# Kernel tuning notes

Hardware: AMD Instinct MI355X
Metric: run time of the kernel (lower is better)

The kernel has to match this reference:

```python
import jax, jax.numpy as jnp
import numpy as np
from jax import lax

N_NODES = 50000
N_EDGES = 1_600_000
BATCH = 4
T_STEPS = 50
DT = 0.02  # integration step (s)


def setup_inputs() -> dict:
    key = jax.random.key(0)
    ks = jax.random.split(key, 8)
    x = jax.random.normal(ks[0], (BATCH, T_STEPS, N_NODES), jnp.float32) * 0.5
    # NeuronBias: normal(mean=0.5, std=0.05)
    bias = (jax.random.normal(ks[1], (N_NODES,), jnp.float32) * 0.05 + 0.5)
    # NeuronTimeConst: around 0.05s, kept positive
    time_const = jax.random.uniform(ks[2], (N_NODES,), jnp.float32) * 0.045 + 0.005
    # EdgeSign: +/-1
    sign = jnp.where(jax.random.uniform(ks[3], (N_EDGES,)) < 0.5, -1.0, 1.0).astype(jnp.float32)
    # SynCount: lognormal, non-negative
    syn_count = jnp.exp(jax.random.normal(ks[4], (N_EDGES,), jnp.float32) * 0.5)
    # SynStrength: small positive scale (scale_chem/scale_elec = 0.01)
    syn_strength = jax.random.uniform(ks[5], (N_EDGES,), jnp.float32) * 0.01
    src_idx = jax.random.randint(ks[6], (N_EDGES,), 0, N_NODES, dtype=jnp.int32)
    tgt_idx = jax.random.randint(ks[7], (N_EDGES,), 0, N_NODES, dtype=jnp.int32)
    return dict(x=x, bias=bias, time_const=time_const, sign=sign,
                syn_count=syn_count, syn_strength=syn_strength,
                src_idx=src_idx, tgt_idx=tgt_idx)


def reference(x, bias, time_const, sign, syn_count, syn_strength, src_idx, tgt_idx):
    """Recurrent connectome dynamics (StaticSynapses, relu activation).

    Per step: gather relu(v) at source nodes, weight each edge by
    sign*syn_count*syn_strength, scatter-add into target nodes, then Euler
    update v += dt/tau * (-v + bias + synaptic_input + stimulus).
    Returns relu(v) over time: [B, T, N].
    """
    B, T, N = x.shape
    # clamp configs: non_negative on counts/strengths
    weight = sign * jax.nn.relu(syn_count) * jax.nn.relu(syn_strength)  # [E]
    tau = jnp.maximum(time_const, DT)
    alpha = DT / tau  # [N]

    v0 = jnp.broadcast_to(bias, (B, N))  # initial state at bias

    def step(v, x_t):
        rates = jax.nn.relu(v)                      # [B, N]
        msg = rates[:, src_idx] * weight            # gather -> edge transform [B, E]
        summed = jnp.zeros((B, N), x.dtype).at[:, tgt_idx].add(msg)  # scatter-reduce
        v_new = v + alpha * (-v + bias + summed + x_t)
        return v_new, jax.nn.relu(v_new)

    _, out = lax.scan(step, v0, jnp.moveaxis(x, 1, 0))  # scan over T
    return jnp.moveaxis(out, 0, 1)  # [B, T, N]
```

## Files before the change

kernel.cpp:

```cpp
#include <hip/hip_runtime.h>
#include <hip/hip_fp16.h>

#define N_NODES 50000
#define N_EDGES 1600000
#define T_STEPS 50
#define DT      0.02f
#define NB      256
#define NPB     196
#define CAP     6912
#define CAP2    7168
#define TILE    4096
#define G       8


__global__ __launch_bounds__(256) void zero_kernel(int* __restrict__ bucket_count) {
    bucket_count[threadIdx.x] = 0;
}

__global__ __launch_bounds__(256) void bucket_kernel(
    const int* __restrict__ src, const int* __restrict__ tgt,
    const float* __restrict__ sign, const float* __restrict__ syn_count,
    const float* __restrict__ syn_strength,
    int* __restrict__ bucket_count, unsigned long long* __restrict__ rec_buf)
{
    __shared__ int hist[NB], base_s[NB], cur[NB];
    int tid = threadIdx.x;
    hist[tid] = 0;
    __syncthreads();

    int e0 = blockIdx.x * TILE + tid;
    int bkt[16];
    unsigned long long item[16];
#pragma unroll
    for (int k = 0; k < 16; ++k) {
        int e = e0 + k * 256;
        if (e < N_EDGES) {
            int t = tgt[e];
            int b = t / NPB;
            int tl = t - b * NPB;
            float w = sign[e] * fmaxf(syn_count[e], 0.f) * fmaxf(syn_strength[e], 0.f);
            unsigned int rec = (unsigned int)src[e] |
                               ((unsigned int)__half_as_ushort(__float2half(w)) << 16);
            bkt[k] = b;
            item[k] = (unsigned long long)rec | ((unsigned long long)tl << 32);
            atomicAdd(&hist[b], 1);
        } else {
            bkt[k] = -1;
        }
    }
    __syncthreads();
    base_s[tid] = atomicAdd(&bucket_count[tid], hist[tid]);
    cur[tid] = 0;
    __syncthreads();
#pragma unroll
    for (int k = 0; k < 16; ++k) {
        if (bkt[k] >= 0) {
            int p = base_s[bkt[k]] + atomicAdd(&cur[bkt[k]], 1);
            if (p < CAP) rec_buf[(size_t)bkt[k] * CAP + p] = item[k];
        }
    }
}

__global__ __launch_bounds__(256) void sort_kernel(
    const int* __restrict__ bucket_count,
    const unsigned long long* __restrict__ rec_buf,
    const float* __restrict__ bias, const float* __restrict__ time_const,
    unsigned int* __restrict__ edges_g,
    int* __restrict__ offsets, int* __restrict__ ends,
    float2* __restrict__ ab, float* __restrict__ v ,
    uint2* __restrict__ rates0 )
{
    __shared__ unsigned int sorted[CAP2];
    __shared__ int loc_off[NPB + 1];
    __shared__ int loc_cnt[NPB];
    __shared__ int loc_cur[NPB];

    int b = blockIdx.x;
    int tid = threadIdx.x;
    int node_base = b * NPB;
    int n_nodes = min(NPB, N_NODES - node_base);
    int ebase = b * CAP2;
    int cnt = min(bucket_count[b], CAP);

    for (int i = tid; i < CAP2; i += 256) sorted[i] = 0;
    if (tid < NPB) loc_cnt[tid] = 0;
    __syncthreads();

    for (int i = tid; i < cnt; i += 256) {
        unsigned long long it = rec_buf[(size_t)b * CAP + i];
        atomicAdd(&loc_cnt[(int)(it >> 32)], 1);
    }
    __syncthreads();
    if (tid == 0) {
        int r = 0;
        for (int n = 0; n < n_nodes; ++n) {
            loc_off[n] = r;
            r += (loc_cnt[n] + 1) & ~1;
        }
        loc_off[n_nodes] = r;
    }
    __syncthreads();
    if (tid < n_nodes) loc_cur[tid] = loc_off[tid];
    __syncthreads();

    for (int i = tid; i < cnt; i += 256) {
        unsigned long long it = rec_buf[(size_t)b * CAP + i];
        int p = atomicAdd(&loc_cur[(int)(it >> 32)], 1);
        sorted[p] = (unsigned int)it;
    }
    __syncthreads();

    int total = loc_off[n_nodes];
    for (int i = tid; i < total; i += 256) edges_g[ebase + i] = sorted[i];
    for (int n = tid; n < n_nodes; n += 256) {
        int gn = node_base + n;
        offsets[gn] = ebase + loc_off[n];
        ends[gn]    = ebase + loc_off[n + 1];
        float bb  = bias[gn];
        float tau = fmaxf(time_const[gn], DT);
        ab[gn] = make_float2(DT / tau, bb);
        v[gn] = bb; v[N_NODES + gn] = bb;
        v[2 * N_NODES + gn] = bb; v[3 * N_NODES + gn] = bb;
        __half hr = __float2half(fmaxf(bb, 0.f));
        __half2 h2 = __halves2half2(hr, hr);
        uint2 r0; r0.x = *(unsigned int*)&h2; r0.y = r0.x;
        rates0[gn] = r0;
    }
}

__device__ __forceinline__ float rec_w(unsigned int rec) {
    return __half2float(__ushort_as_half((unsigned short)(rec >> 16)));
}
__device__ __forceinline__ float4 h4_to_f4(uint2 g) {
    __half2 h01 = *(__half2*)&g.x;
    __half2 h23 = *(__half2*)&g.y;
    float2 f01 = __half22float2(h01);
    float2 f23 = __half22float2(h23);
    return make_float4(f01.x, f01.y, f23.x, f23.y);
}

__global__ __launch_bounds__(256) void step_kernel(
    const uint2* __restrict__ rates_in ,
    __half* __restrict__ rates_out ,
    float* __restrict__ v ,
    const float2* __restrict__ ab,
    const int* __restrict__ offsets, const int* __restrict__ ends,
    const unsigned int* __restrict__ edges,
    const float* __restrict__ x, float* __restrict__ out, int t, int nblk)
{
    int nb8 = nblk / 8;
    int idx = blockIdx.x;
    int node_block = (idx < nb8 * 8) ? (idx % 8) * nb8 + idx / 8 : idx;
    int node = node_block * (256 / G) + ((int)threadIdx.x / G);
    int lane = threadIdx.x & (G - 1);
    if (node >= N_NODES) return;

    int beg = offsets[node], end = ends[node];
    float4 acc = make_float4(0.f, 0.f, 0.f, 0.f);

    const uint2 zz = make_uint2(0u, 0u);
    int i = beg + 2 * lane;
    uint2 p0 = (i          < end) ? *(const uint2*)(edges + i)          : zz;
    uint2 p1 = (i + 2 * G  < end) ? *(const uint2*)(edges + i + 2 * G)  : zz;
    while (i < end) {
        uint2 q0 = (i + 4 * G < end) ? *(const uint2*)(edges + i + 4 * G) : zz;
        uint2 q1 = (i + 6 * G < end) ? *(const uint2*)(edges + i + 6 * G) : zz;
        float4 a0 = h4_to_f4(rates_in[p0.x & 0xFFFFu]);
        float4 a1 = h4_to_f4(rates_in[p0.y & 0xFFFFu]);
        float4 a2 = h4_to_f4(rates_in[p1.x & 0xFFFFu]);
        float4 a3 = h4_to_f4(rates_in[p1.y & 0xFFFFu]);
        float w0 = rec_w(p0.x), w1 = rec_w(p0.y), w2 = rec_w(p1.x), w3 = rec_w(p1.y);
        acc.x = fmaf(a0.x, w0, acc.x); acc.y = fmaf(a0.y, w0, acc.y);
        acc.z = fmaf(a0.z, w0, acc.z); acc.w = fmaf(a0.w, w0, acc.w);
        acc.x = fmaf(a1.x, w1, acc.x); acc.y = fmaf(a1.y, w1, acc.y);
        acc.z = fmaf(a1.z, w1, acc.z); acc.w = fmaf(a1.w, w1, acc.w);
        acc.x = fmaf(a2.x, w2, acc.x); acc.y = fmaf(a2.y, w2, acc.y);
        acc.z = fmaf(a2.z, w2, acc.z); acc.w = fmaf(a2.w, w2, acc.w);
        acc.x = fmaf(a3.x, w3, acc.x); acc.y = fmaf(a3.y, w3, acc.y);
        acc.z = fmaf(a3.z, w3, acc.z); acc.w = fmaf(a3.w, w3, acc.w);
        p0 = q0; p1 = q1;
        i += 4 * G;
    }

#pragma unroll
    for (int m = 1; m < G; m <<= 1) {
        acc.x += __shfl_xor(acc.x, m, 64);
        acc.y += __shfl_xor(acc.y, m, 64);
        acc.z += __shfl_xor(acc.z, m, 64);
        acc.w += __shfl_xor(acc.w, m, 64);
    }

    if (lane < 4) {
        float sum = (lane == 0) ? acc.x : (lane == 1) ? acc.y
                  : (lane == 2) ? acc.z : acc.w;
        float2 abv = ab[node];
        const int TN = T_STEPS * N_NODES;
        int vi = lane * N_NODES + node;
        int oi = lane * TN + t * N_NODES + node;
        float vv = v[vi];
        float xv = __builtin_nontemporal_load(x + oi);
        float vn = vv + abv.x * (abv.y + sum + xv - vv);
        v[vi] = vn;
        float r = fmaxf(vn, 0.f);
        rates_out[node * 4 + lane] = __float2half(r);
        __builtin_nontemporal_store(r, out + oi);
    }
}


extern "C" void kernel_launch(void* const* d_in, const int* in_sizes, int n_in,
                              void* d_out, int out_size, void* d_ws, size_t ws_size,
                              hipStream_t stream) {
    const float* x            = (const float*)d_in[0];
    const float* bias         = (const float*)d_in[1];
    const float* time_const   = (const float*)d_in[2];
    const float* sign         = (const float*)d_in[3];
    const float* syn_count    = (const float*)d_in[4];
    const float* syn_strength = (const float*)d_in[5];
    const int*   src_idx      = (const int*)d_in[6];
    const int*   tgt_idx      = (const int*)d_in[7];
    float* out = (float*)d_out;

    char* ws = (char*)d_ws;
    size_t off = 0;
    auto alloc = [&](size_t bytes) -> void* {
        void* p = ws + off;
        off = (off + bytes + 255) & ~(size_t)255;
        return p;
    };
    float*  v       = (float*) alloc((size_t)N_NODES * 4 * 4);
    uint2*  rates_a = (uint2*) alloc((size_t)N_NODES * 8);
    uint2*  rates_b = (uint2*) alloc((size_t)N_NODES * 8);
    float2* ab      = (float2*)alloc((size_t)N_NODES * 8);
    int*    offsets = (int*)   alloc((size_t)N_NODES * 4);
    int*    ends    = (int*)   alloc((size_t)N_NODES * 4);
    int*    bucket_count = (int*)alloc((size_t)NB * 4);
    unsigned int* edges = (unsigned int*)alloc((size_t)NB * CAP2 * 4);
    unsigned long long* rec_buf =
        (unsigned long long*)alloc((size_t)NB * CAP * 8);

    int nb_tiles = (N_EDGES + TILE - 1) / TILE;

    zero_kernel<<<1, 256, 0, stream>>>(bucket_count);
    bucket_kernel<<<nb_tiles, 256, 0, stream>>>(src_idx, tgt_idx, sign, syn_count,
                                                syn_strength, bucket_count, rec_buf);
    sort_kernel<<<NB, 256, 0, stream>>>(bucket_count, rec_buf, bias, time_const,
                                        edges, offsets, ends, ab, v, rates_a);

    int nblk = (N_NODES + (256 / G) - 1) / (256 / G);
    for (int t = 0; t < T_STEPS; ++t) {
        const uint2* rin  = (t & 1) ? rates_b : rates_a;
        __half*      rout = (__half*)((t & 1) ? rates_a : rates_b);
        step_kernel<<<nblk, 256, 0, stream>>>(rin, rout, v, ab,
                                              offsets, ends, edges, x, out, t, nblk);
    }
}
```

Measured before the change: 788.9 us.

## Stage source-rate chunks in LDS and sort edges by source chunk per node

The sort pass now groups each target node's edges by source-node chunk (8 chunks of 6250 nodes) and records per-chunk offsets. The step kernel becomes 256 blocks of 1024 threads, each with 4 lanes per node. Each block streams the rate array chunk by chunk into shared memory, with register double-buffering, and gathers from LDS instead of global memory. This swaps random global gathers for coalesced loads, but every block reloads the full rate array each step, adds many barriers, and leaves only 256 blocks with little parallelism per node.

```diff
diff --git a/kernel.cpp b/kernel.cpp
--- a/kernel.cpp
+++ b/kernel.cpp
@@ -8,9 +8,10 @@
 #define NB      256
 #define NPB     196
 #define CAP     6912
-#define CAP2    7168
 #define TILE    4096
-#define G       8
+#define NCH     8
+#define CHUNK   6250
+#define SREG    7
 
 
 __global__ __launch_bounds__(256) void zero_kernel(int* __restrict__ bucket_count) {
@@ -65,57 +66,57 @@
     const int* __restrict__ bucket_count,
     const unsigned long long* __restrict__ rec_buf,
     const float* __restrict__ bias, const float* __restrict__ time_const,
-    unsigned int* __restrict__ edges_g,
-    int* __restrict__ offsets, int* __restrict__ ends,
+    unsigned int* __restrict__ edges_g, int* __restrict__ co,
     float2* __restrict__ ab, float* __restrict__ v ,
     uint2* __restrict__ rates0 )
 {
-    __shared__ unsigned int sorted[CAP2];
-    __shared__ int loc_off[NPB + 1];
-    __shared__ int loc_cnt[NPB];
-    __shared__ int loc_cur[NPB];
-
-    int b = blockIdx.x;
-    int tid = threadIdx.x;
+    __shared__ unsigned int sorted[CAP];
+    __shared__ int kcnt[NPB * NCH];
+    __shared__ int kcur[NPB * NCH];
+    __shared__ int nsum[256];
+
+    int b = blockIdx.x, tid = threadIdx.x;
     int node_base = b * NPB;
     int n_nodes = min(NPB, N_NODES - node_base);
-    int ebase = b * CAP2;
+    int ebase = b * CAP;
     int cnt = min(bucket_count[b], CAP);
 
-    for (int i = tid; i < CAP2; i += 256) sorted[i] = 0;
-    if (tid < NPB) loc_cnt[tid] = 0;
+    for (int i = tid; i < NPB * NCH; i += 256) kcnt[i] = 0;
     __syncthreads();
 
     for (int i = tid; i < cnt; i += 256) {
         unsigned long long it = rec_buf[(size_t)b * CAP + i];
-        atomicAdd(&loc_cnt[(int)(it >> 32)], 1);
-    }
-    __syncthreads();
-    if (tid == 0) {
-        int r = 0;
-        for (int n = 0; n < n_nodes; ++n) {
-            loc_off[n] = r;
-            r += (loc_cnt[n] + 1) & ~1;
-        }
-        loc_off[n_nodes] = r;
-    }
-    __syncthreads();
-    if (tid < n_nodes) loc_cur[tid] = loc_off[tid];
-    __syncthreads();
-
-    for (int i = tid; i < cnt; i += 256) {
-        unsigned long long it = rec_buf[(size_t)b * CAP + i];
-        int p = atomicAdd(&loc_cur[(int)(it >> 32)], 1);
-        sorted[p] = (unsigned int)it;
-    }
-    __syncthreads();
-
-    int total = loc_off[n_nodes];
-    for (int i = tid; i < total; i += 256) edges_g[ebase + i] = sorted[i];
-    for (int n = tid; n < n_nodes; n += 256) {
-        int gn = node_base + n;
-        offsets[gn] = ebase + loc_off[n];
-        ends[gn]    = ebase + loc_off[n + 1];
+        int tl = (int)(it >> 32);
+        int c  = (int)((unsigned int)it & 0xFFFFu) / CHUNK;
+        atomicAdd(&kcnt[tl * NCH + c], 1);
+    }
+    __syncthreads();
+
+    int my_tot = 0;
+    if (tid < NPB) {
+#pragma unroll
+        for (int k = 0; k < NCH; ++k) my_tot += kcnt[tid * NCH + k];
+    }
+    nsum[tid] = my_tot;
+    __syncthreads();
+    for (int off = 1; off < 256; off <<= 1) {
+        int val = (tid >= off) ? nsum[tid - off] : 0;
+        __syncthreads();
+        nsum[tid] += val;
+        __syncthreads();
+    }
+
+    if (tid < n_nodes) {
+        int run = (tid == 0) ? 0 : nsum[tid - 1];
+        int gn = node_base + tid;
+#pragma unroll
+        for (int k = 0; k < NCH; ++k) {
+            kcur[tid * NCH + k] = run;
+            co[gn * (NCH + 1) + k] = ebase + run;
+            run += kcnt[tid * NCH + k];
+        }
+        co[gn * (NCH + 1) + NCH] = ebase + run;
+
         float bb  = bias[gn];
         float tau = fmaxf(time_const[gn], DT);
         ab[gn] = make_float2(DT / tau, bb);
@@ -126,6 +127,18 @@
         uint2 r0; r0.x = *(unsigned int*)&h2; r0.y = r0.x;
         rates0[gn] = r0;
     }
+    __syncthreads();
+
+    for (int i = tid; i < cnt; i += 256) {
+        unsigned long long it = rec_buf[(size_t)b * CAP + i];
+        int tl = (int)(it >> 32);
+        int c  = (int)((unsigned int)it & 0xFFFFu) / CHUNK;
+        int p = atomicAdd(&kcur[tl * NCH + c], 1);
+        sorted[p] = (unsigned int)it;
+    }
+    __syncthreads();
+
+    for (int i = tid; i < cnt; i += 256) edges_g[ebase + i] = sorted[i];
 }
 
 __device__ __forceinline__ float rec_w(unsigned int rec) {
@@ -139,71 +152,96 @@
     return make_float4(f01.x, f01.y, f23.x, f23.y);
 }
 
-__global__ __launch_bounds__(256) void step_kernel(
+__global__ __launch_bounds__(1024) void step_kernel(
     const uint2* __restrict__ rates_in ,
     __half* __restrict__ rates_out ,
     float* __restrict__ v ,
     const float2* __restrict__ ab,
-    const int* __restrict__ offsets, const int* __restrict__ ends,
-    const unsigned int* __restrict__ edges,
-    const float* __restrict__ x, float* __restrict__ out, int t, int nblk)
+    const int* __restrict__ co, const unsigned int* __restrict__ edges,
+    const float* __restrict__ x, float* __restrict__ out, int t)
 {
-    int nb8 = nblk / 8;
-    int idx = blockIdx.x;
-    int node_block = (idx < nb8 * 8) ? (idx % 8) * nb8 + idx / 8 : idx;
-    int node = node_block * (256 / G) + ((int)threadIdx.x / G);
-    int lane = threadIdx.x & (G - 1);
-    if (node >= N_NODES) return;
-
-    int beg = offsets[node], end = ends[node];
+    __shared__ uint2 lds_r[CHUNK];
+
+    int b = blockIdx.x, tid = threadIdx.x;
+    int node_base = b * NPB;
+    int n_nodes = min(NPB, N_NODES - node_base);
+    int group = tid >> 2, lane = tid & 3;
+    bool active = group < n_nodes;
+    int gn = node_base + group;
     float4 acc = make_float4(0.f, 0.f, 0.f, 0.f);
 
-    const uint2 zz = make_uint2(0u, 0u);
-    int i = beg + 2 * lane;
-    uint2 p0 = (i          < end) ? *(const uint2*)(edges + i)          : zz;
-    uint2 p1 = (i + 2 * G  < end) ? *(const uint2*)(edges + i + 2 * G)  : zz;
-    while (i < end) {
-        uint2 q0 = (i + 4 * G < end) ? *(const uint2*)(edges + i + 4 * G) : zz;
-        uint2 q1 = (i + 6 * G < end) ? *(const uint2*)(edges + i + 6 * G) : zz;
-        float4 a0 = h4_to_f4(rates_in[p0.x & 0xFFFFu]);
-        float4 a1 = h4_to_f4(rates_in[p0.y & 0xFFFFu]);
-        float4 a2 = h4_to_f4(rates_in[p1.x & 0xFFFFu]);
-        float4 a3 = h4_to_f4(rates_in[p1.y & 0xFFFFu]);
-        float w0 = rec_w(p0.x), w1 = rec_w(p0.y), w2 = rec_w(p1.x), w3 = rec_w(p1.y);
+    int off9[NCH + 1];
+    if (active) {
+#pragma unroll
+        for (int k = 0; k <= NCH; ++k) off9[k] = co[gn * (NCH + 1) + k];
+    } else {
+#pragma unroll
+        for (int k = 0; k <= NCH; ++k) off9[k] = 0;
+    }
+
+    uint2 st[SREG];
+#pragma unroll
+    for (int k = 0; k < SREG; ++k) {
+        int i = tid + k * 1024;
+        st[k] = (i < CHUNK) ? rates_in[i] : make_uint2(0u, 0u);
+    }
+
+    for (int c = 0; c < NCH; ++c) {
+        __syncthreads();
+#pragma unroll
+        for (int k = 0; k < SREG; ++k) {
+            int i = tid + k * 1024;
+            if (i < CHUNK) lds_r[i] = st[k];
+        }
+        if (c + 1 < NCH) {
+            const uint2* nxt = rates_in + (c + 1) * CHUNK;
+#pragma unroll
+            for (int k = 0; k < SREG; ++k) {
+                int i = tid + k * 1024;
+                st[k] = (i < CHUNK) ? nxt[i] : make_uint2(0u, 0u);
+            }
+        }
+        __syncthreads();
+
+        int beg = off9[c], end = off9[c + 1];
+        int cb = c * CHUNK;
+        int i = beg + lane;
+        unsigned int r0 = (i     < end) ? edges[i]     : (unsigned int)cb;
+        unsigned int r1 = (i + 4 < end) ? edges[i + 4] : (unsigned int)cb;
+        float4 a0 = h4_to_f4(lds_r[(int)(r0 & 0xFFFFu) - cb]);
+        float4 a1 = h4_to_f4(lds_r[(int)(r1 & 0xFFFFu) - cb]);
+        float w0 = rec_w(r0), w1 = rec_w(r1);
         acc.x = fmaf(a0.x, w0, acc.x); acc.y = fmaf(a0.y, w0, acc.y);
         acc.z = fmaf(a0.z, w0, acc.z); acc.w = fmaf(a0.w, w0, acc.w);
         acc.x = fmaf(a1.x, w1, acc.x); acc.y = fmaf(a1.y, w1, acc.y);
         acc.z = fmaf(a1.z, w1, acc.z); acc.w = fmaf(a1.w, w1, acc.w);
-        acc.x = fmaf(a2.x, w2, acc.x); acc.y = fmaf(a2.y, w2, acc.y);
-        acc.z = fmaf(a2.z, w2, acc.z); acc.w = fmaf(a2.w, w2, acc.w);
-        acc.x = fmaf(a3.x, w3, acc.x); acc.y = fmaf(a3.y, w3, acc.y);
-        acc.z = fmaf(a3.z, w3, acc.z); acc.w = fmaf(a3.w, w3, acc.w);
-        p0 = q0; p1 = q1;
-        i += 4 * G;
-    }
-
-#pragma unroll
-    for (int m = 1; m < G; m <<= 1) {
-        acc.x += __shfl_xor(acc.x, m, 64);
-        acc.y += __shfl_xor(acc.y, m, 64);
-        acc.z += __shfl_xor(acc.z, m, 64);
-        acc.w += __shfl_xor(acc.w, m, 64);
-    }
-
-    if (lane < 4) {
+        for (i += 8; i < end; i += 4) {
+            unsigned int rr = edges[i];
+            float ww = rec_w(rr);
+            float4 ar = h4_to_f4(lds_r[(int)(rr & 0xFFFFu) - cb]);
+            acc.x = fmaf(ar.x, ww, acc.x); acc.y = fmaf(ar.y, ww, acc.y);
+            acc.z = fmaf(ar.z, ww, acc.z); acc.w = fmaf(ar.w, ww, acc.w);
+        }
+    }
+
+    acc.x += __shfl_xor(acc.x, 1, 64); acc.y += __shfl_xor(acc.y, 1, 64);
+    acc.z += __shfl_xor(acc.z, 1, 64); acc.w += __shfl_xor(acc.w, 1, 64);
+    acc.x += __shfl_xor(acc.x, 2, 64); acc.y += __shfl_xor(acc.y, 2, 64);
+    acc.z += __shfl_xor(acc.z, 2, 64); acc.w += __shfl_xor(acc.w, 2, 64);
+
+    if (active) {
         float sum = (lane == 0) ? acc.x : (lane == 1) ? acc.y
                   : (lane == 2) ? acc.z : acc.w;
-        float2 abv = ab[node];
+        float2 abv = ab[gn];
         const int TN = T_STEPS * N_NODES;
-        int vi = lane * N_NODES + node;
-        int oi = lane * TN + t * N_NODES + node;
+        int vi = lane * N_NODES + gn;
+        int oi = lane * TN + t * N_NODES + gn;
         float vv = v[vi];
-        float xv = __builtin_nontemporal_load(x + oi);
-        float vn = vv + abv.x * (abv.y + sum + xv - vv);
+        float vn = vv + abv.x * (abv.y + sum + x[oi] - vv);
         v[vi] = vn;
         float r = fmaxf(vn, 0.f);
-        rates_out[node * 4 + lane] = __float2half(r);
-        __builtin_nontemporal_store(r, out + oi);
+        rates_out[gn * 4 + lane] = __float2half(r);
+        out[oi] = r;
     }
 }
 
@@ -232,10 +270,9 @@
     uint2*  rates_a = (uint2*) alloc((size_t)N_NODES * 8);
     uint2*  rates_b = (uint2*) alloc((size_t)N_NODES * 8);
     float2* ab      = (float2*)alloc((size_t)N_NODES * 8);
-    int*    offsets = (int*)   alloc((size_t)N_NODES * 4);
-    int*    ends    = (int*)   alloc((size_t)N_NODES * 4);
+    int*    co      = (int*)   alloc((size_t)N_NODES * (NCH + 1) * 4);
     int*    bucket_count = (int*)alloc((size_t)NB * 4);
-    unsigned int* edges = (unsigned int*)alloc((size_t)NB * CAP2 * 4);
+    unsigned int* edges = (unsigned int*)alloc((size_t)NB * CAP * 4);
     unsigned long long* rec_buf =
         (unsigned long long*)alloc((size_t)NB * CAP * 8);
 
@@ -245,13 +282,12 @@
     bucket_kernel<<<nb_tiles, 256, 0, stream>>>(src_idx, tgt_idx, sign, syn_count,
                                                 syn_strength, bucket_count, rec_buf);
     sort_kernel<<<NB, 256, 0, stream>>>(bucket_count, rec_buf, bias, time_const,
-                                        edges, offsets, ends, ab, v, rates_a);
-
-    int nblk = (N_NODES + (256 / G) - 1) / (256 / G);
+                                        edges, co, ab, v, rates_a);
+
     for (int t = 0; t < T_STEPS; ++t) {
         const uint2* rin  = (t & 1) ? rates_b : rates_a;
         __half*      rout = (__half*)((t & 1) ? rates_a : rates_b);
-        step_kernel<<<nblk, 256, 0, stream>>>(rin, rout, v, ab,
-                                              offsets, ends, edges, x, out, t, nblk);
-    }
-}
+        step_kernel<<<NB, 1024, 0, stream>>>(rin, rout, v, ab, co, edges,
+                                             x, out, t);
+    }
+}
```

Result: slower. 879.7 us (+11.5%).
